# Optimization experiments

Measured on AMD Instinct MI355X. Metric: run time of the kernel, lower is better.

Reference implementation:

```python
import jax, jax.numpy as jnp
import numpy as np

B, L, N_PATCH, NUM_Q, C_IN, C_OUT = 32, 40, 2304, 100, 768, 256


def setup_inputs() -> dict:
    key = jax.random.key(0)
    ks = jax.random.split(key, 7)
    text_feat = jax.random.normal(ks[0], (B, L, C_IN), jnp.float32)
    img_feat = jax.random.normal(ks[1], (B, N_PATCH, C_IN), jnp.float32)
    # text_scores in (0,1): scale fns use log(1.22 - x), valid for x < 1.22
    text_scores = jax.random.uniform(ks[2], (B, 1), jnp.float32, 0.01, 0.99)
    text_mask = jax.random.randint(ks[3], (B, L), 0, 2).astype(jnp.int32)
    # guarantee at least a few unmasked text tokens per row (avoid all -inf)
    text_mask = text_mask.at[:, :4].set(0)
    dummy_token = jax.random.normal(ks[4], (1, NUM_Q, C_IN), jnp.float32)
    Wq = jax.random.normal(ks[5], (C_OUT, C_IN), jnp.float32) / np.sqrt(C_IN).astype(np.float32)
    bq = jnp.zeros((C_OUT,), jnp.float32)
    return dict(text_feat=text_feat, img_feat=img_feat, text_scores=text_scores,
                text_mask=text_mask, dummy_token=dummy_token, Wq=Wq, bq=bq)


def _l2norm(x, eps=1e-8):
    n = jnp.linalg.norm(x, axis=-1, keepdims=True)
    return x / jnp.maximum(n, eps)


def reference(text_feat, img_feat, text_scores, text_mask, dummy_token, Wq, bq):
    b, n_patch, c = img_feat.shape
    num_q = dummy_token.shape[1]
    l = text_feat.shape[1]

    # img features with learned dummy tokens appended: [B, N+Q, C]
    img_all = jnp.concatenate(
        [img_feat, jnp.broadcast_to(dummy_token, (b, num_q, c))], axis=1)

    # cosine similarity between every (patch|dummy) and every text token: [B, N+Q, L]
    cos = jnp.einsum('bpc,blc->bpl', _l2norm(img_all), _l2norm(text_feat))
    sim_norm = (cos + 1.0) * 0.5

    # custom log-based scale factors from text confidence score ([B,1])
    log_term = jnp.log(1.22 - text_scores)            # [B, 1]
    not_dummy = -0.59 * log_term + 0.12               # applied to real patches
    dummy = 0.59 * log_term + 0.88                    # applied to dummy tokens
    scale_factor = jnp.concatenate(
        [jnp.broadcast_to(not_dummy[:, :, None], (b, n_patch, l)),
         jnp.broadcast_to(dummy[:, :, None], (b, num_q, l))], axis=1)

    scaled = scale_factor * sim_norm                  # [B, N+Q, L]
    scaled = jnp.where(text_mask[:, None, :].astype(bool), -jnp.inf, scaled)

    # masked max over text tokens, then topk over patches (+dummies)
    max_per_patch = jnp.max(scaled, axis=-1)          # [B, N+Q]
    _, topk_idx = jax.lax.top_k(max_per_patch, num_q)  # [B, Q]

    # gather selected features (equivalent to one-hot scatter + bmm in torch)
    selected = jnp.take_along_axis(img_all, topk_idx[:, :, None], axis=1)  # [B,Q,C]
    query = selected @ Wq.T + bq                      # [B, Q, C_OUT]
    return query, topk_idx, sim_norm, scaled
```

## Files before the change

### kernel.cpp

```cpp
#include <hip/hip_runtime.h>
#include <math.h>

#define B_    32
#define L_    40
#define PIMG  2304
#define NQ    100
#define PALL  2404
#define C_    768
#define COUT  256
#define NT    24
#define TP    64

#define NEG_INF (-__builtin_huge_valf())
#define MASK_SENTINEL (-3.0e38f)

typedef short s16x8 __attribute__((ext_vector_type(8)));
typedef float f32x4 __attribute__((ext_vector_type(4)));

#define BSTR 40

__device__ __forceinline__ unsigned cvtpk(float a, float b) {
    unsigned r;
    asm("v_cvt_pk_bf16_f32 %0, %1, %2" : "=v"(r) : "v"(a), "v"(b));
    return r;
}
__device__ __forceinline__ void cvt44u(float4 v, uint2* h, uint2* l) {
    unsigned h01 = cvtpk(v.x, v.y);
    unsigned h23 = cvtpk(v.z, v.w);
    *h = make_uint2(h01, h23);
    *l = make_uint2(
        cvtpk(v.x - __uint_as_float(h01 << 16), v.y - __uint_as_float(h01 & 0xFFFF0000u)),
        cvtpk(v.z - __uint_as_float(h23 << 16), v.w - __uint_as_float(h23 & 0xFFFF0000u)));
}
union U4S8 { uint4 u; s16x8 s; };
__device__ __forceinline__ void split8(float4 v0, float4 v1, s16x8& h, s16x8& l) {
    unsigned h0 = cvtpk(v0.x, v0.y);
    unsigned h1 = cvtpk(v0.z, v0.w);
    unsigned h2 = cvtpk(v1.x, v1.y);
    unsigned h3 = cvtpk(v1.z, v1.w);
    unsigned l0 = cvtpk(v0.x - __uint_as_float(h0 << 16), v0.y - __uint_as_float(h0 & 0xFFFF0000u));
    unsigned l1 = cvtpk(v0.z - __uint_as_float(h1 << 16), v0.w - __uint_as_float(h1 & 0xFFFF0000u));
    unsigned l2 = cvtpk(v1.x - __uint_as_float(h2 << 16), v1.y - __uint_as_float(h2 & 0xFFFF0000u));
    unsigned l3 = cvtpk(v1.z - __uint_as_float(h3 << 16), v1.w - __uint_as_float(h3 & 0xFFFF0000u));
    U4S8 uh; uh.u = make_uint4(h0, h1, h2, h3); h = uh.s;
    U4S8 ul; ul.u = make_uint4(l0, l1, l2, l3); l = ul.s;
}
__device__ __forceinline__ float dot4(float4 v) {
    return v.x * v.x + v.y * v.y + v.z * v.z + v.w * v.w;
}

__device__ __forceinline__ void gl16(const float* g, float* lds_base) {
#if __has_builtin(__builtin_amdgcn_global_load_lds)
    __builtin_amdgcn_global_load_lds(
        (const __attribute__((address_space(1))) void*)g,
        (__attribute__((address_space(3))) void*)lds_base, 16, 0, 0);
#else
    const int lane = threadIdx.x & 63;
    *(float4*)((char*)lds_base + lane * 16) = *(const float4*)g;
#endif
}

#define MFMA3(ACC, AH, AL, BH, BL) \
    ACC = __builtin_amdgcn_mfma_f32_16x16x32_bf16(AH, BH, ACC, 0, 0, 0); \
    ACC = __builtin_amdgcn_mfma_f32_16x16x32_bf16(AH, BL, ACC, 0, 0, 0); \
    ACC = __builtin_amdgcn_mfma_f32_16x16x32_bf16(AL, BH, ACC, 0, 0, 0);

__global__ void k_scales(const float* __restrict__ scores,
                         float* __restrict__ sA, float* __restrict__ sB) {
    int t = threadIdx.x;
    if (t < B_) {
        float s  = scores[t];
        float lt = logf(1.22f - s);
        sA[t] = -0.59f * lt + 0.12f;
        sB[t] =  0.59f * lt + 0.88f;
    }
}

__global__ void k_textnorm(const float* __restrict__ text, float* __restrict__ invT) {
    int t    = threadIdx.x;
    int row  = blockIdx.x * 4 + (t >> 6);
    int lane = t & 63;
    const float* src = text + (size_t)row * C_;
    float ss = 0.f;
#pragma unroll
    for (int j = 0; j < 12; ++j) {
        float x = src[lane + 64 * j];
        ss += x * x;
    }
#pragma unroll
    for (int m = 1; m < 64; m <<= 1) ss += __shfl_xor(ss, m);
    if (lane == 0) invT[row] = 1.0f / fmaxf(sqrtf(ss), 1e-8f);
}

__global__ __launch_bounds__(256) void k_main(
    const float* __restrict__ img,  const float* __restrict__ dummy,
    const float* __restrict__ text, const float* __restrict__ invT,
    const int*  __restrict__ mask,  const float* __restrict__ scaleA,
    const float* __restrict__ scaleB, float* __restrict__ simn,
    float* __restrict__ scld, float* __restrict__ maxpp)
{
    __shared__ float  Af[2][TP * 32];
    __shared__ ushort Bh[2][L_][BSTR], Bl[2][L_][BSTR];
    __shared__ float  invT_s[48];
    __shared__ int    mask_s[48];

    const int t    = threadIdx.x;
    const int b    = blockIdx.y;
    const int p0   = blockIdx.x * TP;
    const int lane = t & 63, w = t >> 6;
    const int lr   = lane & 15, kg = lane >> 4;

    if (t < 48) {
        invT_s[t] = (t < L_) ? invT[b * L_ + t] : 0.f;
        mask_s[t] = (t < L_) ? mask[b * L_ + t] : 1;
    }

    const float sA = scaleA[b], sB = scaleB[b];

    const int drow = lane >> 3, dchk = lane & 7;
    const int r0 = w * 16 + drow, r1 = r0 + 8;
    const int g0 = dchk ^ (r0 & 7), g1 = dchk ^ (r1 & 7);
    const int pA0 = min(p0 + r0, PALL - 1), pA1 = min(p0 + r1, PALL - 1);
    const float* gp0 = ((pA0 < PIMG) ? img + ((size_t)b * PIMG + pA0) * C_
                                     : dummy + (size_t)(pA0 - PIMG) * C_) + g0 * 4;
    const float* gp1 = ((pA1 < PIMG) ? img + ((size_t)b * PIMG + pA1) * C_
                                     : dummy + (size_t)(pA1 - PIMG) * C_) + g1 * 4;

    const int bl = t >> 2, bq = t & 3;
    const float* bbase = (t < 160) ? text + ((size_t)b * L_ + bl) * C_ + bq * 8 : nullptr;

    f32x4 acc[3];
#pragma unroll
    for (int ct = 0; ct < 3; ++ct) acc[ct] = (f32x4){0.f, 0.f, 0.f, 0.f};
    float nrm = 0.f;

    auto STAGE_A = [&](int it, int buf) {
        gl16(gp0 + it * 32, &Af[buf][(w * 16) * 32]);
        gl16(gp1 + it * 32, &Af[buf][(w * 16 + 8) * 32]);
    };
    auto LOADB = [&](int it, float4& v0, float4& v1) {
        if (bbase) {
            v0 = *(const float4*)(bbase + it * 32);
            v1 = *(const float4*)(bbase + it * 32 + 4);
        }
    };
    auto STOREB = [&](int buf, float4 v0, float4 v1) {
        if (bbase) {
            uint2 h, l;
            cvt44u(v0, &h, &l);
            { int q = bq * 2,     c = (q & 3) * 8 + (q >> 2) * 4;
              *(uint2*)&Bh[buf][bl][c] = h; *(uint2*)&Bl[buf][bl][c] = l; }
            cvt44u(v1, &h, &l);
            { int q = bq * 2 + 1, c = (q & 3) * 8 + (q >> 2) * 4;
              *(uint2*)&Bh[buf][bl][c] = h; *(uint2*)&Bl[buf][bl][c] = l; }
        }
    };
    auto COMPUTE = [&](int buf) {
        const int row = w * 16 + lr;
        const char* arow = (const char*)&Af[buf][row * 32];
        const int sw8 = row & 7;
        float4 va0 = *(const float4*)(arow + ((kg ^ sw8) << 4));
        float4 va1 = *(const float4*)(arow + (((4 + kg) ^ sw8) << 4));
        nrm += dot4(va0) + dot4(va1);
        s16x8 ah, al;
        split8(va0, va1, ah, al);
#pragma unroll
        for (int ct = 0; ct < 3; ++ct) {
            const int brow = min(ct * 16 + lr, L_ - 1);
            s16x8 bh  = *(const s16x8*)&Bh[buf][brow][kg * 8];
            s16x8 blo = *(const s16x8*)&Bl[buf][brow][kg * 8];
            MFMA3(acc[ct], ah, al, bh, blo);
        }
    };

    float4 xb0, xb1, yb0, yb1;
    STAGE_A(0, 0);
    LOADB(0, xb0, xb1);
    STOREB(0, xb0, xb1);
    LOADB(1, yb0, yb1);
    __syncthreads();

    for (int it = 0; it < NT; it += 2) {
        if (it + 1 < NT) { STAGE_A(it + 1, 1); STOREB(1, yb0, yb1); }
        if (it + 2 < NT) LOADB(it + 2, xb0, xb1);
        COMPUTE(0);
        __syncthreads();

        if (it + 2 < NT) { STAGE_A(it + 2, 0); STOREB(0, xb0, xb1); }
        if (it + 3 < NT) LOADB(it + 3, yb0, yb1);
        if (it + 1 < NT) COMPUTE(1);
        __syncthreads();
    }

    nrm += __shfl_xor(nrm, 16);
    nrm += __shfl_xor(nrm, 32);

#pragma unroll
    for (int reg = 0; reg < 4; ++reg) {
        const float ss   = __shfl(nrm, kg * 4 + reg);
        const float invn = 1.f / fmaxf(sqrtf(ss), 1e-8f);
        const int rloc = w * 16 + kg * 4 + reg;
        const int pp   = p0 + rloc;
        float mrow = NEG_INF;
        if (pp < PALL) {
            const float scl = (pp < PIMG) ? sA : sB;
            const size_t obase = ((size_t)b * PALL + pp) * L_;
#pragma unroll
            for (int ct = 0; ct < 3; ++ct) {
                const int col = ct * 16 + lr;
                float cosv = acc[ct][reg] * invn * invT_s[col];
                float sim  = (cosv + 1.f) * 0.5f;
                float sc   = mask_s[col] ? MASK_SENTINEL : scl * sim;
                if (col < L_) {
                    simn[obase + col] = sim;
                    scld[obase + col] = sc;
                    mrow = fmaxf(mrow, sc);
                }
            }
        }
        mrow = fmaxf(mrow, __shfl_xor(mrow, 1));
        mrow = fmaxf(mrow, __shfl_xor(mrow, 2));
        mrow = fmaxf(mrow, __shfl_xor(mrow, 4));
        mrow = fmaxf(mrow, __shfl_xor(mrow, 8));
        if (lr == 0 && pp < PALL) maxpp[b * PALL + pp] = mrow;
    }
}

__global__ __launch_bounds__(256) void k_rank(const float* __restrict__ maxpp,
                                              int* __restrict__ tki,
                                              float* __restrict__ topkf)
{
    __shared__ unsigned long long keys[PALL] __attribute__((aligned(16)));
    const int t = threadIdx.x;
    const int b = blockIdx.y;
    const int base = blockIdx.x * 512;
    const float* src = maxpp + (size_t)b * PALL;

    for (int i = t; i < PALL; i += 256) {
        unsigned u = __float_as_uint(src[i]);
        u = (u & 0x80000000u) ? ~u : (u | 0x80000000u);
        keys[i] = ((unsigned long long)u << 32) | (unsigned)(~i);
    }
    __syncthreads();

    const int i0 = base + t, i1 = base + t + 256;
    const unsigned long long k0 = (i0 < PALL) ? keys[i0] : ~0ull;
    const unsigned long long k1 = (i1 < PALL) ? keys[i1] : ~0ull;
    int c0 = 0, c1 = 0;
#pragma unroll 8
    for (int j = 0; j < PALL; j += 2) {
        ulonglong2 kk = *(const ulonglong2*)&keys[j];
        c0 += (kk.x > k0); c0 += (kk.y > k0);
        c1 += (kk.x > k1); c1 += (kk.y > k1);
    }
    if (i0 < PALL && c0 < NQ) { tki[b * NQ + c0] = i0; topkf[b * NQ + c0] = (float)i0; }
    if (i1 < PALL && c1 < NQ) { tki[b * NQ + c1] = i1; topkf[b * NQ + c1] = (float)i1; }
}

__global__ __launch_bounds__(256) void k_query(
    const float* __restrict__ img, const float* __restrict__ dummy,
    const float* __restrict__ Wq,  const float* __restrict__ bqv,
    const int*  __restrict__ tki,  float* __restrict__ query)
{
    __shared__ ushort Ah[2][64][BSTR], Al[2][64][BSTR];
    __shared__ ushort Bh[2][32][BSTR], Bl[2][32][BSTR];
    __shared__ const float* rowp[64];

    const int t    = threadIdx.x, lane = t & 63, w = t >> 6;
    const int lr   = lane & 15, kg = lane >> 4;
    const int rb   = blockIdx.x * 64, cb = blockIdx.y * 32;

    if (t < 64) {
        int R = rb + t; int sel = tki[R]; int bb = R / NQ;
        rowp[t] = (sel < PIMG) ? img + ((size_t)bb * PIMG + sel) * C_
                               : dummy + (size_t)(sel - PIMG) * C_;
    }
    __syncthreads();

    const int sr = t >> 2, sh = t & 3;
    const float* abase = rowp[sr] + sh * 8;
    const float* bbase = (t < 128) ? Wq + (size_t)(cb + (t >> 2)) * C_ + (t & 3) * 8 : nullptr;
    const int bl = t >> 2, bq = t & 3;

    f32x4 acc[2];
#pragma unroll
    for (int ct = 0; ct < 2; ++ct) acc[ct] = (f32x4){0.f, 0.f, 0.f, 0.f};

#define LOADQ(IT, A0, A1, Bv0, Bv1) do { \
        const int k0_ = (IT) * 32; \
        A0 = *(const float4*)(abase + k0_); \
        A1 = *(const float4*)(abase + k0_ + 4); \
        if (bbase) { \
            Bv0 = *(const float4*)(bbase + k0_); \
            Bv1 = *(const float4*)(bbase + k0_ + 4); \
        } \
    } while (0)

    auto STORE = [&](ushort (*AhD)[BSTR], ushort (*AlD)[BSTR],
                     ushort (*BhD)[BSTR], ushort (*BlD)[BSTR],
                     float4 A0, float4 A1, float4 Bv0, float4 Bv1) {
        uint2 h, l;
        cvt44u(A0, &h, &l);
        {
            const int q = sh * 2, col = (q & 3) * 8 + (q >> 2) * 4;
            *(uint2*)&AhD[sr][col] = h; *(uint2*)&AlD[sr][col] = l;
        }
        cvt44u(A1, &h, &l);
        {
            const int q = sh * 2 + 1, col = (q & 3) * 8 + (q >> 2) * 4;
            *(uint2*)&AhD[sr][col] = h; *(uint2*)&AlD[sr][col] = l;
        }
        if (bbase) {
            cvt44u(Bv0, &h, &l);
            {
                const int q = bq * 2, col = (q & 3) * 8 + (q >> 2) * 4;
                *(uint2*)&BhD[bl][col] = h; *(uint2*)&BlD[bl][col] = l;
            }
            cvt44u(Bv1, &h, &l);
            {
                const int q = bq * 2 + 1, col = (q & 3) * 8 + (q >> 2) * 4;
                *(uint2*)&BhD[bl][col] = h; *(uint2*)&BlD[bl][col] = l;
            }
        }
    };
    auto COMPUTE = [&](ushort (*AhS)[BSTR], ushort (*AlS)[BSTR],
                       ushort (*BhS)[BSTR], ushort (*BlS)[BSTR]) {
        const int row = w * 16 + lr;
        s16x8 ah = *(const s16x8*)&AhS[row][kg * 8];
        s16x8 al = *(const s16x8*)&AlS[row][kg * 8];
#pragma unroll
        for (int ct = 0; ct < 2; ++ct) {
            s16x8 bh  = *(const s16x8*)&BhS[ct * 16 + lr][kg * 8];
            s16x8 blo = *(const s16x8*)&BlS[ct * 16 + lr][kg * 8];
            MFMA3(acc[ct], ah, al, bh, blo);
        }
    };

    float4 xa0, xa1, xb0, xb1, ya0, ya1, yb0, yb1;
    LOADQ(0, xa0, xa1, xb0, xb1);
    STORE(Ah[0], Al[0], Bh[0], Bl[0], xa0, xa1, xb0, xb1);
    __syncthreads();

    for (int it = 0; it < NT; it += 2) {
        LOADQ(it + 1, ya0, ya1, yb0, yb1);
        COMPUTE(Ah[0], Al[0], Bh[0], Bl[0]);
        STORE(Ah[1], Al[1], Bh[1], Bl[1], ya0, ya1, yb0, yb1);
        __syncthreads();

        if (it + 2 < NT) LOADQ(it + 2, xa0, xa1, xb0, xb1);
        COMPUTE(Ah[1], Al[1], Bh[1], Bl[1]);
        if (it + 2 < NT) STORE(Ah[0], Al[0], Bh[0], Bl[0], xa0, xa1, xb0, xb1);
        __syncthreads();
    }
#undef LOADQ

#pragma unroll
    for (int reg = 0; reg < 4; ++reg) {
        const int R = rb + w * 16 + kg * 4 + reg;
#pragma unroll
        for (int ct = 0; ct < 2; ++ct) {
            const int col = cb + ct * 16 + lr;
            query[(size_t)R * COUT + col] = acc[ct][reg] + bqv[col];
        }
    }
}

extern "C" void kernel_launch(void* const* d_in, const int* in_sizes, int n_in,
                              void* d_out, int out_size, void* d_ws, size_t ws_size,
                              hipStream_t stream) {
    const float* text   = (const float*)d_in[0];
    const float* img    = (const float*)d_in[1];
    const float* scores = (const float*)d_in[2];
    const int*   mask   = (const int*)  d_in[3];
    const float* dummy  = (const float*)d_in[4];
    const float* Wq     = (const float*)d_in[5];
    const float* bq     = (const float*)d_in[6];

    float* out   = (float*)d_out;
    float* query = out;
    float* topkf = out + 819200;
    float* simn  = out + 822400;
    float* scld  = out + 3899520;

    float* wsf   = (float*)d_ws;
    float* invT  = wsf;
    float* sA    = wsf + 1280;
    float* sB    = wsf + 1312;
    float* maxpp = wsf + 1344;
    int*   tki   = (int*)(wsf + 78272);

    hipLaunchKernelGGL(k_scales,   dim3(1),      dim3(64),  0, stream, scores, sA, sB);
    hipLaunchKernelGGL(k_textnorm, dim3(320),    dim3(256), 0, stream, text, invT);
    hipLaunchKernelGGL(k_main,     dim3(38, 32), dim3(256), 0, stream,
                       img, dummy, text, invT, mask, sA, sB, simn, scld, maxpp);
    hipLaunchKernelGGL(k_rank,     dim3(5, 32),  dim3(256), 0, stream, maxpp, tki, topkf);
    hipLaunchKernelGGL(k_query,    dim3(50, 8),  dim3(256), 0, stream,
                       img, dummy, Wq, bq, tki, query);
}
```

Baseline: 133.3 us.

## Pre-split text into bf16 hi/lo in textnorm; load main-loop operands directly to registers

The text-norm kernel now also writes bf16 hi/lo splits of the text features in a permuted layout matching the MFMA B-operand order. The main kernel drops all LDS staging and barriers. Each lane loads its A row fragment and the pre-split B fragments straight from global memory into registers, double-buffered in software. This removes per-block LDS traffic, repeated conversion of text, and __syncthreads. The cost is redundant global and L2 reads of text across the four waves and all blocks, plus extra register pressure from the two register buffers.

```diff
diff --git a/kernel.cpp b/kernel.cpp
--- a/kernel.cpp
+++ b/kernel.cpp
@@ -23,6 +23,14 @@
     unsigned r;
     asm("v_cvt_pk_bf16_f32 %0, %1, %2" : "=v"(r) : "v"(a), "v"(b));
     return r;
+}
+__device__ __forceinline__ ushort f2bf(float x) {
+    unsigned u = __float_as_uint(x);
+    u = u + 0x7FFFu + ((u >> 16) & 1u);
+    return (ushort)(u >> 16);
+}
+__device__ __forceinline__ float bf2f(ushort h) {
+    return __uint_as_float(((unsigned)h) << 16);
 }
 __device__ __forceinline__ void cvt44u(float4 v, uint2* h, uint2* l) {
     unsigned h01 = cvtpk(v.x, v.y);
@@ -49,17 +57,6 @@
     return v.x * v.x + v.y * v.y + v.z * v.z + v.w * v.w;
 }
 
-__device__ __forceinline__ void gl16(const float* g, float* lds_base) {
-#if __has_builtin(__builtin_amdgcn_global_load_lds)
-    __builtin_amdgcn_global_load_lds(
-        (const __attribute__((address_space(1))) void*)g,
-        (__attribute__((address_space(3))) void*)lds_base, 16, 0, 0);
-#else
-    const int lane = threadIdx.x & 63;
-    *(float4*)((char*)lds_base + lane * 16) = *(const float4*)g;
-#endif
-}
-
 #define MFMA3(ACC, AH, AL, BH, BL) \
     ACC = __builtin_amdgcn_mfma_f32_16x16x32_bf16(AH, BH, ACC, 0, 0, 0); \
     ACC = __builtin_amdgcn_mfma_f32_16x16x32_bf16(AH, BL, ACC, 0, 0, 0); \
@@ -76,16 +73,26 @@
     }
 }
 
-__global__ void k_textnorm(const float* __restrict__ text, float* __restrict__ invT) {
+__global__ void k_textnorm(const float* __restrict__ text, float* __restrict__ invT,
+                           ushort* __restrict__ th, ushort* __restrict__ tl) {
     int t    = threadIdx.x;
     int row  = blockIdx.x * 4 + (t >> 6);
     int lane = t & 63;
     const float* src = text + (size_t)row * C_;
+    ushort* dh = th + (size_t)row * C_;
+    ushort* dl = tl + (size_t)row * C_;
     float ss = 0.f;
 #pragma unroll
     for (int j = 0; j < 12; ++j) {
-        float x = src[lane + 64 * j];
+        int   k = lane + 64 * j;
+        float x = src[k];
         ss += x * x;
+        ushort hi = f2bf(x);
+        ushort lo = f2bf(x - bf2f(hi));
+        int kw = k & 31;
+        int kp = (k & ~31) + 8 * ((kw >> 2) & 3) + 4 * ((kw >> 4) & 1) + (kw & 3);
+        dh[kp] = hi;
+        dl[kp] = lo;
     }
 #pragma unroll
     for (int m = 1; m < 64; m <<= 1) ss += __shfl_xor(ss, m);
@@ -94,103 +101,79 @@
 
 __global__ __launch_bounds__(256) void k_main(
     const float* __restrict__ img,  const float* __restrict__ dummy,
-    const float* __restrict__ text, const float* __restrict__ invT,
-    const int*  __restrict__ mask,  const float* __restrict__ scaleA,
-    const float* __restrict__ scaleB, float* __restrict__ simn,
-    float* __restrict__ scld, float* __restrict__ maxpp)
+    const ushort* __restrict__ th,  const ushort* __restrict__ tl,
+    const float* __restrict__ invT, const int*  __restrict__ mask,
+    const float* __restrict__ scaleA, const float* __restrict__ scaleB,
+    float* __restrict__ simn, float* __restrict__ scld,
+    float* __restrict__ maxpp)
 {
-    __shared__ float  Af[2][TP * 32];
-    __shared__ ushort Bh[2][L_][BSTR], Bl[2][L_][BSTR];
-    __shared__ float  invT_s[48];
-    __shared__ int    mask_s[48];
-
     const int t    = threadIdx.x;
     const int b    = blockIdx.y;
     const int p0   = blockIdx.x * TP;
     const int lane = t & 63, w = t >> 6;
     const int lr   = lane & 15, kg = lane >> 4;
 
-    if (t < 48) {
-        invT_s[t] = (t < L_) ? invT[b * L_ + t] : 0.f;
-        mask_s[t] = (t < L_) ? mask[b * L_ + t] : 1;
-    }
-
     const float sA = scaleA[b], sB = scaleB[b];
 
-    const int drow = lane >> 3, dchk = lane & 7;
-    const int r0 = w * 16 + drow, r1 = r0 + 8;
-    const int g0 = dchk ^ (r0 & 7), g1 = dchk ^ (r1 & 7);
-    const int pA0 = min(p0 + r0, PALL - 1), pA1 = min(p0 + r1, PALL - 1);
-    const float* gp0 = ((pA0 < PIMG) ? img + ((size_t)b * PIMG + pA0) * C_
-                                     : dummy + (size_t)(pA0 - PIMG) * C_) + g0 * 4;
-    const float* gp1 = ((pA1 < PIMG) ? img + ((size_t)b * PIMG + pA1) * C_
-                                     : dummy + (size_t)(pA1 - PIMG) * C_) + g1 * 4;
-
-    const int bl = t >> 2, bq = t & 3;
-    const float* bbase = (t < 160) ? text + ((size_t)b * L_ + bl) * C_ + bq * 8 : nullptr;
+    const int row = w * 16 + lr;
+    const int pA  = min(p0 + row, PALL - 1);
+    const float* abase =
+        ((pA < PIMG) ? img + ((size_t)b * PIMG + pA) * C_
+                     : dummy + (size_t)(pA - PIMG) * C_) + kg * 4;
+
+    const ushort* thb = th + (size_t)b * L_ * C_;
+    const ushort* tlb = tl + (size_t)b * L_ * C_;
+    const size_t bo0 = (size_t)lr * C_ + kg * 8;
+    const size_t bo1 = (size_t)(16 + lr) * C_ + kg * 8;
+    const size_t bo2 = (size_t)min(32 + lr, L_ - 1) * C_ + kg * 8;
+    const ushort* bh0p = thb + bo0; const ushort* bl0p = tlb + bo0;
+    const ushort* bh1p = thb + bo1; const ushort* bl1p = tlb + bo1;
+    const ushort* bh2p = thb + bo2; const ushort* bl2p = tlb + bo2;
+
+    float invTv[3]; int maskv[3];
+#pragma unroll
+    for (int ct = 0; ct < 3; ++ct) {
+        int col = ct * 16 + lr;
+        invTv[ct] = (col < L_) ? invT[b * L_ + col] : 0.f;
+        maskv[ct] = (col < L_) ? mask[b * L_ + col] : 1;
+    }
 
     f32x4 acc[3];
 #pragma unroll
     for (int ct = 0; ct < 3; ++ct) acc[ct] = (f32x4){0.f, 0.f, 0.f, 0.f};
     float nrm = 0.f;
 
-    auto STAGE_A = [&](int it, int buf) {
-        gl16(gp0 + it * 32, &Af[buf][(w * 16) * 32]);
-        gl16(gp1 + it * 32, &Af[buf][(w * 16 + 8) * 32]);
+#define LOADT(IT, A0, A1, B0, B1, B2, B3, B4, B5) do { \
+        const int ko_ = (IT) * 32; \
+        A0 = *(const float4*)(abase + ko_); \
+        A1 = *(const float4*)(abase + ko_ + 16); \
+        B0 = *(const s16x8*)(bh0p + ko_); B1 = *(const s16x8*)(bl0p + ko_); \
+        B2 = *(const s16x8*)(bh1p + ko_); B3 = *(const s16x8*)(bl1p + ko_); \
+        B4 = *(const s16x8*)(bh2p + ko_); B5 = *(const s16x8*)(bl2p + ko_); \
+    } while (0)
+
+    auto TILE = [&](float4 A0, float4 A1, s16x8 B0, s16x8 B1, s16x8 B2,
+                    s16x8 B3, s16x8 B4, s16x8 B5) {
+        nrm += dot4(A0) + dot4(A1);
+        s16x8 ah, al;
+        split8(A0, A1, ah, al);
+        MFMA3(acc[0], ah, al, B0, B1);
+        MFMA3(acc[1], ah, al, B2, B3);
+        MFMA3(acc[2], ah, al, B4, B5);
     };
-    auto LOADB = [&](int it, float4& v0, float4& v1) {
-        if (bbase) {
-            v0 = *(const float4*)(bbase + it * 32);
-            v1 = *(const float4*)(bbase + it * 32 + 4);
-        }
-    };
-    auto STOREB = [&](int buf, float4 v0, float4 v1) {
-        if (bbase) {
-            uint2 h, l;
-            cvt44u(v0, &h, &l);
-            { int q = bq * 2,     c = (q & 3) * 8 + (q >> 2) * 4;
-              *(uint2*)&Bh[buf][bl][c] = h; *(uint2*)&Bl[buf][bl][c] = l; }
-            cvt44u(v1, &h, &l);
-            { int q = bq * 2 + 1, c = (q & 3) * 8 + (q >> 2) * 4;
-              *(uint2*)&Bh[buf][bl][c] = h; *(uint2*)&Bl[buf][bl][c] = l; }
-        }
-    };
-    auto COMPUTE = [&](int buf) {
-        const int row = w * 16 + lr;
-        const char* arow = (const char*)&Af[buf][row * 32];
-        const int sw8 = row & 7;
-        float4 va0 = *(const float4*)(arow + ((kg ^ sw8) << 4));
-        float4 va1 = *(const float4*)(arow + (((4 + kg) ^ sw8) << 4));
-        nrm += dot4(va0) + dot4(va1);
-        s16x8 ah, al;
-        split8(va0, va1, ah, al);
-#pragma unroll
-        for (int ct = 0; ct < 3; ++ct) {
-            const int brow = min(ct * 16 + lr, L_ - 1);
-            s16x8 bh  = *(const s16x8*)&Bh[buf][brow][kg * 8];
-            s16x8 blo = *(const s16x8*)&Bl[buf][brow][kg * 8];
-            MFMA3(acc[ct], ah, al, bh, blo);
-        }
-    };
-
-    float4 xb0, xb1, yb0, yb1;
-    STAGE_A(0, 0);
-    LOADB(0, xb0, xb1);
-    STOREB(0, xb0, xb1);
-    LOADB(1, yb0, yb1);
-    __syncthreads();
-
+
+    float4 xa0, xa1, ya0, ya1;
+    s16x8  xb0, xb1, xb2, xb3, xb4, xb5;
+    s16x8  yb0, yb1, yb2, yb3, yb4, yb5;
+    LOADT(0, xa0, xa1, xb0, xb1, xb2, xb3, xb4, xb5);
     for (int it = 0; it < NT; it += 2) {
-        if (it + 1 < NT) { STAGE_A(it + 1, 1); STOREB(1, yb0, yb1); }
-        if (it + 2 < NT) LOADB(it + 2, xb0, xb1);
-        COMPUTE(0);
-        __syncthreads();
-
-        if (it + 2 < NT) { STAGE_A(it + 2, 0); STOREB(0, xb0, xb1); }
-        if (it + 3 < NT) LOADB(it + 3, yb0, yb1);
-        if (it + 1 < NT) COMPUTE(1);
-        __syncthreads();
-    }
+        LOADT(it + 1, ya0, ya1, yb0, yb1, yb2, yb3, yb4, yb5);
+        TILE(xa0, xa1, xb0, xb1, xb2, xb3, xb4, xb5);
+        if (it + 2 < NT)
+            LOADT(it + 2, xa0, xa1, xb0, xb1, xb2, xb3, xb4, xb5);
+        TILE(ya0, ya1, yb0, yb1, yb2, yb3, yb4, yb5);
+    }
+#undef LOADT
 
     nrm += __shfl_xor(nrm, 16);
     nrm += __shfl_xor(nrm, 32);
@@ -208,9 +191,9 @@
 #pragma unroll
             for (int ct = 0; ct < 3; ++ct) {
                 const int col = ct * 16 + lr;
-                float cosv = acc[ct][reg] * invn * invT_s[col];
+                float cosv = acc[ct][reg] * invn * invTv[ct];
                 float sim  = (cosv + 1.f) * 0.5f;
-                float sc   = mask_s[col] ? MASK_SENTINEL : scl * sim;
+                float sc   = maskv[ct] ? MASK_SENTINEL : scl * sim;
                 if (col < L_) {
                     simn[obase + col] = sim;
                     scld[obase + col] = sc;
@@ -388,11 +371,13 @@
     float* sB    = wsf + 1312;
     float* maxpp = wsf + 1344;
     int*   tki   = (int*)(wsf + 78272);
+    ushort* th   = (ushort*)(wsf + 81472);
+    ushort* tl   = th + (size_t)B_ * L_ * C_;
 
     hipLaunchKernelGGL(k_scales,   dim3(1),      dim3(64),  0, stream, scores, sA, sB);
-    hipLaunchKernelGGL(k_textnorm, dim3(320),    dim3(256), 0, stream, text, invT);
+    hipLaunchKernelGGL(k_textnorm, dim3(320),    dim3(256), 0, stream, text, invT, th, tl);
     hipLaunchKernelGGL(k_main,     dim3(38, 32), dim3(256), 0, stream,
-                       img, dummy, text, invT, mask, sA, sB, simn, scld, maxpp);
+                       img, dummy, th, tl, invT, mask, sA, sB, simn, scld, maxpp);
     hipLaunchKernelGGL(k_rank,     dim3(5, 32),  dim3(256), 0, stream, maxpp, tki, topkf);
     hipLaunchKernelGGL(k_query,    dim3(50, 8),  dim3(256), 0, stream,
                        img, dummy, Wq, bq, tki, query);
```

Result: slower. 192.9 us (+44.7%).
